# Performance work log

Measured on AMD Instinct MI355X. Metric: run time of the kernel, lower is better.

Reference implementation:

```python
import jax, jax.numpy as jnp
import numpy as np

DIM = 384
H_RES, W_RES = 56, 56
HEADS = 12
WS = 7          # window size
SS = 3          # shift size
N = WS * WS     # tokens per window
NW = (H_RES // WS) * (W_RES // WS)
EPS = 1e-5


def _rel_pos_index(ws):
    coords = np.stack(np.meshgrid(np.arange(ws), np.arange(ws), indexing='ij'))  # [2,ws,ws]
    cf = coords.reshape(2, -1)                      # [2, N]
    rc = (cf[:, :, None] - cf[:, None, :]).transpose(1, 2, 0)  # [N,N,2]
    rc[..., 0] += ws - 1
    rc[..., 1] += ws - 1
    rc[..., 0] *= 2 * ws - 1
    return rc.sum(-1)                               # [N,N] int


def _attn_mask(h, w, ws, ss):
    img = np.zeros((h, w))
    cnt = 0
    slices = (slice(0, -ws), slice(-ws, -ss), slice(-ss, None))
    for hs in slices:
        for wsl in slices:
            img[hs, wsl] = cnt
            cnt += 1
    mw = img.reshape(h // ws, ws, w // ws, ws).transpose(0, 2, 1, 3).reshape(-1, ws * ws)  # [nW,N]
    d = mw[:, None, :] - mw[:, :, None]
    return np.where(d != 0, -100.0, 0.0).astype(np.float32)  # [nW,N,N]


RPI = jnp.asarray(_rel_pos_index(WS).reshape(-1))          # [N*N]
ATTN_MASK = jnp.asarray(_attn_mask(H_RES, W_RES, WS, SS))  # [nW,N,N]


def _layernorm(x, g, b):
    mu = jnp.mean(x, axis=-1, keepdims=True)
    var = jnp.mean(jnp.square(x - mu), axis=-1, keepdims=True)
    return (x - mu) * jax.lax.rsqrt(var + EPS) * g + b


def setup_inputs() -> dict:
    key = jax.random.key(0)
    ks = jax.random.split(key, 8)
    s = 0.02
    return {
        'x': jax.random.normal(ks[0], (32, 1 + H_RES * W_RES, DIM), jnp.float32),
        'norm1_g': jnp.ones((DIM,), jnp.float32),
        'norm1_b': jnp.zeros((DIM,), jnp.float32),
        'qkv_w': jax.random.normal(ks[1], (DIM, 3 * DIM), jnp.float32) * s,
        'qkv_b': jnp.zeros((3 * DIM,), jnp.float32),
        'rpb_table': jax.random.normal(ks[2], ((2 * WS - 1) ** 2, HEADS), jnp.float32) * s,
        'proj_w': jax.random.normal(ks[3], (DIM, DIM), jnp.float32) * s,
        'proj_b': jnp.zeros((DIM,), jnp.float32),
        'norm2_g': jnp.ones((DIM,), jnp.float32),
        'norm2_b': jnp.zeros((DIM,), jnp.float32),
        'fc1_w': jax.random.normal(ks[4], (DIM, 4 * DIM), jnp.float32) * s,
        'fc1_b': jnp.zeros((4 * DIM,), jnp.float32),
        'fc2_w': jax.random.normal(ks[5], (4 * DIM, DIM), jnp.float32) * s,
        'fc2_b': jnp.zeros((DIM,), jnp.float32),
    }


def reference(x, norm1_g, norm1_b, qkv_w, qkv_b, rpb_table, proj_w, proj_b,
              norm2_g, norm2_b, fc1_w, fc1_b, fc2_w, fc2_b):
    B = x.shape[0]
    C = DIM
    hd = C // HEADS
    scale = hd ** -0.5

    time_token = x[:, :1, :]          # [B,1,C]
    img = x[:, 1:, :]                 # [B,H*W,C]
    shortcut = img

    h = _layernorm(img, norm1_g, norm1_b).reshape(B, H_RES, W_RES, C)
    h = jnp.roll(h, shift=(-SS, -SS), axis=(1, 2))  # cyclic shift

    # window partition -> [B*nW, N, C]
    xw = h.reshape(B, H_RES // WS, WS, W_RES // WS, WS, C)
    xw = xw.transpose(0, 1, 3, 2, 4, 5).reshape(-1, N, C)

    # window attention
    qkv = (xw @ qkv_w + qkv_b).reshape(-1, N, 3, HEADS, hd).transpose(2, 0, 3, 1, 4)
    q, k, v = qkv[0], qkv[1], qkv[2]                 # [B*nW, H, N, hd]
    attn = jnp.einsum('whnd,whmd->whnm', q * scale, k)
    bias = rpb_table[RPI].reshape(N, N, HEADS).transpose(2, 0, 1)  # [H,N,N]
    attn = attn + bias[None]
    attn = attn.reshape(B, NW, HEADS, N, N) + ATTN_MASK[None, :, None]
    attn = jax.nn.softmax(attn.reshape(-1, HEADS, N, N), axis=-1)
    out = jnp.einsum('whnm,whmd->wnhd', attn, v).reshape(-1, N, C)
    out = out @ proj_w + proj_b

    # window reverse -> [B,H,W,C]
    out = out.reshape(B, H_RES // WS, W_RES // WS, WS, WS, C)
    out = out.transpose(0, 1, 3, 2, 4, 5).reshape(B, H_RES, W_RES, C)
    out = jnp.roll(out, shift=(SS, SS), axis=(1, 2)).reshape(B, H_RES * W_RES, C)

    img = shortcut + out
    x = jnp.concatenate([time_token, img], axis=1)   # [B,1+H*W,C]
    x = _layernorm(x, norm2_g, norm2_b)
    hmlp = jax.nn.gelu(x @ fc1_w + fc1_b, approximate=False)
    x = x + (hmlp @ fc2_w + fc2_b)
    return x
```

## Files before the change

### kernel.cpp

```cpp
#include <hip/hip_runtime.h>
#include <hip/hip_bf16.h>

#define DIM 384
#define HEADS 12
#define NTOK 49
#define TOKENS 3137
#define M_ATTN 100352
#define M_FULL 100384
#define M_PAD  100480
#define SCALEQ 0.17677669529663687f

typedef __attribute__((ext_vector_type(8))) short s8v;
typedef __attribute__((ext_vector_type(4))) float f4v;
typedef unsigned short u16;

__device__ __forceinline__ float b2f(int s) {
  union { unsigned u; float f; } c; c.u = ((unsigned)(s & 0xffff)) << 16; return c.f;
}
__device__ __forceinline__ u16 f2b(float f) {
  __hip_bfloat16 h = __float2bfloat16(f);
  return *reinterpret_cast<u16*>(&h);
}
__device__ __forceinline__ void gload16(const void* g, void* l) {
  __builtin_amdgcn_global_load_lds((const __attribute__((address_space(1))) void*)g,
                                   (__attribute__((address_space(3))) void*)l, 16, 0, 0);
}
__device__ __forceinline__ float gelu_f(float val) {
  float u = __builtin_fmaf(0.0713548163f * val, val * val, 1.5957691216f * val);
  return val * __builtin_amdgcn_rcpf(1.0f + __expf(-u));
}
__device__ __forceinline__ size_t tidx(int tile, int KS, int rl, int c) {
  return ((size_t)(tile * KS + (c >> 6)) * 128 + rl) * 64
       + (((((c >> 3) & 7)) ^ (rl & 7)) << 3) + (c & 7);
}

__global__ void k_convert(const float* __restrict__ qkv_w, const float* __restrict__ qkv_b,
                          const float* __restrict__ proj_w, const float* __restrict__ fc1_w,
                          const float* __restrict__ fc2_w,
                          u16* __restrict__ wt_qkv, float* __restrict__ qkvb_s,
                          u16* __restrict__ wt_proj, u16* __restrict__ wt_fc1,
                          u16* __restrict__ wt_fc2) {
  int i = blockIdx.x * 256 + threadIdx.x;
  if (i < 1152 * 384) { int n = i / 384, k = i % 384;
    float v = qkv_w[(size_t)k * 1152 + n]; if (n < 384) v *= SCALEQ;
    wt_qkv[tidx(n >> 7, 6, n & 127, k)] = f2b(v); }
  if (i < 1152) qkvb_s[i] = qkv_b[i] * (i < 384 ? SCALEQ : 1.0f);
  if (i < 384 * 384) { int n = i / 384, k = i % 384;
    wt_proj[tidx(n >> 7, 6, n & 127, k)] = f2b(proj_w[(size_t)k * 384 + n]); }
  if (i < 1536 * 384) { int n = i / 384, k = i % 384;
    wt_fc1[tidx(n >> 7, 6, n & 127, k)] = f2b(fc1_w[(size_t)k * 1536 + n]); }
  if (i < 384 * 1536) { int n = i / 1536, k = i % 1536;
    wt_fc2[tidx(n >> 7, 24, n & 127, k)] = f2b(fc2_w[(size_t)k * 384 + n]); }
}

__global__ void k_addtab(const float* __restrict__ rpb, float* __restrict__ ADD) {
  int idx = blockIdx.x * 256 + threadIdx.x;
  if (idx >= 4 * HEADS * NTOK * NTOK) return;
  int j = idx % NTOK, t = idx / NTOK;
  int i = t % NTOK; t /= NTOK;
  int h = t % HEADS; int cls = t / HEADS;
  int ii = i / 7, jj = i % 7, ji = j / 7, j2 = j % 7;
  int rpi = (ii - ji + 6) * 13 + (jj - j2 + 6);
  float v = rpb[rpi * HEADS + h];
  int rh = (cls & 2) ? (ii < 4 ? 1 : 2) : 0;
  int rw = (cls & 1) ? (jj < 4 ? 1 : 2) : 0;
  int sh = (cls & 2) ? (ji < 4 ? 1 : 2) : 0;
  int sw = (cls & 1) ? (j2 < 4 ? 1 : 2) : 0;
  if (rh != sh || rw != sw) v -= 100.0f;
  ADD[idx] = v;
}

__global__ void k_ln1(const float* __restrict__ x, const float* __restrict__ g,
                      const float* __restrict__ b, u16* __restrict__ xwt, int t0) {
  int wid = threadIdx.x >> 6, lane = threadIdx.x & 63;
  int ml = blockIdx.x * 4 + wid;
  int t = t0 + ml;
  int bi = t / 3136, rem = t % 3136;
  int win = rem / NTOK, n = rem % NTOK;
  int wh = win >> 3, ww = win & 7, ii = n / 7, jj = n % 7;
  int h = (wh * 7 + ii + 3) % 56;
  int w = (ww * 7 + jj + 3) % 56;
  const float* src = x + ((size_t)bi * TOKENS + 1 + h * 56 + w) * DIM;
  float v[6];
  #pragma unroll
  for (int e = 0; e < 6; e++) v[e] = src[lane + e * 64];
  float s = v[0] + v[1] + v[2] + v[3] + v[4] + v[5];
  #pragma unroll
  for (int m = 1; m < 64; m <<= 1) s += __shfl_xor(s, m);
  float mu = s * (1.0f / 384.0f);
  float q = 0.f;
  #pragma unroll
  for (int e = 0; e < 6; e++) { float d = v[e] - mu; q += d * d; }
  #pragma unroll
  for (int m = 1; m < 64; m <<= 1) q += __shfl_xor(q, m);
  float rstd = rsqrtf(q * (1.0f / 384.0f) + 1e-5f);
  int tile = ml >> 7, rl = ml & 127;
  #pragma unroll
  for (int e = 0; e < 6; e++) {
    int c = lane + e * 64;
    xwt[tidx(tile, 6, rl, c)] = f2b((v[e] - mu) * rstd * g[c] + b[c]);
  }
}

template<int MODE>
__global__ __launch_bounds__(256) void k_gemm(
    const u16* __restrict__ At, const u16* __restrict__ Bt,
    const float* __restrict__ bias, u16* __restrict__ Cb,
    float* __restrict__ outp, const u16* __restrict__ residt,
    int N, int KT, int row_off) {
  __shared__ __align__(16) u16 As[2][128 * 64];
  __shared__ __align__(16) u16 Bs[2][128 * 64];
  int gx = gridDim.x;
  int lid = blockIdx.y * gx + blockIdx.x;
  int nwg = gx * gridDim.y;
  int q = nwg >> 3, r = nwg & 7;
  int xcd = lid & 7, loc = lid >> 3;
  int tile = (xcd < r ? xcd * (q + 1) : r * (q + 1) + (xcd - r) * q) + loc;
  int m0 = (tile / gx) * 128, n0 = (tile % gx) * 128;
  int t = threadIdx.x;
  int lane = t & 63, wave = t >> 6;
  int lo = lane & 15, hi = lane >> 4;
  int wr = (wave >> 1) * 64, wc = (wave & 1) * 64;
  const u16* Ag = At + ((size_t)(m0 >> 7) * KT) * 8192 + wave * 2048 + lane * 8;
  const u16* Bg = Bt + ((size_t)(n0 >> 7) * KT) * 8192 + wave * 2048 + lane * 8;
  f4v acc[4][4];
  #pragma unroll
  for (int m = 0; m < 4; m++)
    #pragma unroll
    for (int n = 0; n < 4; n++) acc[m][n] = (f4v)(0.0f);
#define STAGE(buf, kt) do {                                              \
    u16* al_ = As[buf] + wave * 2048;                                    \
    u16* bl_ = Bs[buf] + wave * 2048;                                    \
    _Pragma("unroll")                                                    \
    for (int g_ = 0; g_ < 4; g_++) {                                     \
      gload16(Ag + (size_t)(kt) * 8192 + g_ * 512, al_ + g_ * 512);      \
      gload16(Bg + (size_t)(kt) * 8192 + g_ * 512, bl_ + g_ * 512);      \
    } } while (0)
  STAGE(0, 0);
  for (int kt = 0; kt < KT; ++kt) {
    int c = kt & 1;
    if (kt + 1 < KT) {
      STAGE(1 - c, kt + 1);
      asm volatile("s_waitcnt vmcnt(8)" ::: "memory");
    } else {
      asm volatile("s_waitcnt vmcnt(0)" ::: "memory");
    }
    __builtin_amdgcn_s_barrier();
    __builtin_amdgcn_sched_barrier(0);
    s8v af[2][4], bfr[2][4];
    #pragma unroll
    for (int kk = 0; kk < 2; kk++) {
      #pragma unroll
      for (int m = 0; m < 4; m++) {
        int row = wr + m * 16 + lo;
        af[kk][m] = *(const s8v*)(As[c] + row * 64 + (((kk * 4 + hi) ^ (row & 7)) * 8));
      }
      #pragma unroll
      for (int n = 0; n < 4; n++) {
        int row = wc + n * 16 + lo;
        bfr[kk][n] = *(const s8v*)(Bs[c] + row * 64 + (((kk * 4 + hi) ^ (row & 7)) * 8));
      }
    }
    asm volatile("s_waitcnt lgkmcnt(0)" ::: "memory");
    __builtin_amdgcn_sched_barrier(0);
    __builtin_amdgcn_s_barrier();
    __builtin_amdgcn_sched_barrier(0);
    __builtin_amdgcn_s_setprio(1);
    #pragma unroll
    for (int kk = 0; kk < 2; kk++)
      #pragma unroll
      for (int m = 0; m < 4; m++)
        #pragma unroll
        for (int n = 0; n < 4; n++)
          acc[m][n] = __builtin_amdgcn_mfma_f32_16x16x32_bf16(af[kk][m], bfr[kk][n], acc[m][n], 0, 0, 0);
    __builtin_amdgcn_s_setprio(0);
  }
#undef STAGE
  #pragma unroll
  for (int m = 0; m < 4; m++) {
    #pragma unroll
    for (int n = 0; n < 4; n++) {
      int gcol = n0 + wc + n * 16 + lo;
      float bv = bias[gcol];
      #pragma unroll
      for (int r2 = 0; r2 < 4; r2++) {
        int lrow = wr + m * 16 + hi * 4 + r2;
        float val = acc[m][n][r2] + bv;
        if (MODE == 0) {
          Cb[(size_t)(m0 + lrow) * N + gcol] = f2b(val);
        } else if (MODE == 1) {
          Cb[tidx(m0 >> 7, 24, lrow, gcol)] = f2b(gelu_f(val));
        } else {
          int orow = m0 + lrow + row_off;
          if (orow < M_FULL) {
            float res = b2f(residt[tidx(orow >> 7, 6, orow & 127, gcol)]);
            outp[(size_t)orow * 384 + gcol] = val + res;
          }
        }
      }
    }
  }
}

__global__ __launch_bounds__(256) void k_attn2(const u16* __restrict__ qkv,
                                               const float* __restrict__ ADD,
                                               u16* __restrict__ aot, int win0) {
  __shared__ u16 PT[4][64][76];
  __shared__ u16 VT[4][32][76];
  int wid = threadIdx.x >> 6, lane = threadIdx.x & 63;
  int lo = lane & 15, hi = lane >> 4;
  int gw = blockIdx.x * 4 + wid;
  int win_l = gw / HEADS, h = gw % HEADS;
  int nw = (win0 + win_l) & 63;
  int wh = nw >> 3, ww = nw & 7;
  int cls = ((wh == 7) ? 2 : 0) + ((ww == 7) ? 1 : 0);
  size_t rowbase = (size_t)win_l * NTOK;
  u16 (*pt)[76] = PT[wid];
  u16 (*vt)[76] = VT[wid];

  int rcl[4];
  #pragma unroll
  for (int ti = 0; ti < 4; ti++) {
    int r = ti * 16 + lo;
    rcl[ti] = r < NTOK ? r : NTOK - 1;
  }
  int jrow = lane < NTOK ? lane : NTOK - 1;

  s8v af[4], bf[4];
  #pragma unroll
  for (int ti = 0; ti < 4; ti++) {
    af[ti] = *(const s8v*)(qkv + (rowbase + rcl[ti]) * 1152 + h * 32 + hi * 8);
    bf[ti] = *(const s8v*)(qkv + (rowbase + rcl[ti]) * 1152 + 384 + h * 32 + hi * 8);
  }
  f4v st[4][4];
  #pragma unroll
  for (int mi = 0; mi < 4; mi++)
    #pragma unroll
    for (int ni = 0; ni < 4; ni++)
      st[mi][ni] = __builtin_amdgcn_mfma_f32_16x16x32_bf16(af[mi], bf[ni], (f4v)(0.0f), 0, 0, 0);

  {
    const u16* vsrc = qkv + (rowbase + jrow) * 1152 + 768 + h * 32;
    #pragma unroll
    for (int d0 = 0; d0 < 32; d0 += 8) {
      s8v v = *(const s8v*)(vsrc + d0);
      #pragma unroll
      for (int e = 0; e < 8; e++) vt[d0 + e][lane] = (u16)v[e];
    }
  }

  const float* addb = ADD + ((size_t)cls * HEADS + h) * (NTOK * NTOK);
  #pragma unroll
  for (int mi = 0; mi < 4; mi++)
    #pragma unroll
    for (int ni = 0; ni < 4; ni++) {
      int jj = ni * 16 + lo;
      #pragma unroll
      for (int r = 0; r < 4; r++) {
        int i = mi * 16 + hi * 4 + r;
        if (jj < NTOK) {
          int ic = i < NTOK ? i : NTOK - 1;
          st[mi][ni][r] += addb[ic * NTOK + jj];
        } else st[mi][ni][r] = -1e30f;
      }
    }

  float invl[4][4];
  #pragma unroll
  for (int mi = 0; mi < 4; mi++)
    #pragma unroll
    for (int r = 0; r < 4; r++) {
      float m = fmaxf(fmaxf(st[mi][0][r], st[mi][1][r]), fmaxf(st[mi][2][r], st[mi][3][r]));
      #pragma unroll
      for (int msk = 1; msk < 16; msk <<= 1) m = fmaxf(m, __shfl_xor(m, msk));
      float s = 0.f;
      #pragma unroll
      for (int ni = 0; ni < 4; ni++) {
        float p = __expf(st[mi][ni][r] - m);
        st[mi][ni][r] = p;
        s += p;
      }
      #pragma unroll
      for (int msk = 1; msk < 16; msk <<= 1) s += __shfl_xor(s, msk);
      invl[mi][r] = 1.0f / s;
    }

  #pragma unroll
  for (int ni = 0; ni < 4; ni++)
    #pragma unroll
    for (int mi = 0; mi < 4; mi++) {
      ushort4 pk;
      pk.x = f2b(st[mi][ni][0]); pk.y = f2b(st[mi][ni][1]);
      pk.z = f2b(st[mi][ni][2]); pk.w = f2b(st[mi][ni][3]);
      *(ushort4*)(&pt[ni * 16 + lo][mi * 16 + hi * 4]) = pk;
    }

  f4v ot[4][2];
  #pragma unroll
  for (int mi = 0; mi < 4; mi++)
    #pragma unroll
    for (int dt = 0; dt < 2; dt++) ot[mi][dt] = (f4v)(0.0f);
  #pragma unroll
  for (int kt = 0; kt < 2; kt++) {
    s8v pa[4], vb[2];
    #pragma unroll
    for (int mi = 0; mi < 4; mi++) {
      s8v p;
      #pragma unroll
      for (int e = 0; e < 8; e++) p[e] = (short)pt[kt * 32 + hi * 8 + e][mi * 16 + lo];
      pa[mi] = p;
    }
    #pragma unroll
    for (int dt = 0; dt < 2; dt++) {
      short4 a = *(const short4*)(&vt[dt * 16 + lo][kt * 32 + hi * 8]);
      short4 b = *(const short4*)(&vt[dt * 16 + lo][kt * 32 + hi * 8 + 4]);
      s8v v; v[0] = a.x; v[1] = a.y; v[2] = a.z; v[3] = a.w;
             v[4] = b.x; v[5] = b.y; v[6] = b.z; v[7] = b.w;
      vb[dt] = v;
    }
    #pragma unroll
    for (int mi = 0; mi < 4; mi++)
      #pragma unroll
      for (int dt = 0; dt < 2; dt++)
        ot[mi][dt] = __builtin_amdgcn_mfma_f32_16x16x32_bf16(pa[mi], vb[dt], ot[mi][dt], 0, 0, 0);
  }

  #pragma unroll
  for (int mi = 0; mi < 4; mi++)
    #pragma unroll
    for (int r = 0; r < 4; r++) {
      int i = mi * 16 + hi * 4 + r;
      if (i < NTOK) {
        int row = (int)rowbase + i;
        int tile = row >> 7, rl = row & 127;
        aot[tidx(tile, 6, rl, h * 32 + lo)]      = f2b(ot[mi][0][r] * invl[mi][r]);
        aot[tidx(tile, 6, rl, h * 32 + 16 + lo)] = f2b(ot[mi][1][r] * invl[mi][r]);
      }
    }
}

__global__ void k_ln2(const float* __restrict__ x, const u16* __restrict__ proj,
                      const float* __restrict__ g, const float* __restrict__ b,
                      u16* __restrict__ x2bt) {
  int wid = threadIdx.x >> 6, lane = threadIdx.x & 63;
  int r = blockIdx.x * 4 + wid;
  int tile = r >> 7, rl = r & 127;
  if (r >= M_FULL) {
    u16 z = f2b(0.0f);
    #pragma unroll
    for (int e = 0; e < 6; e++) x2bt[tidx(tile, 6, rl, lane + e * 64)] = z;
    return;
  }
  int bi = r / TOKENS, tk = r % TOKENS;
  const float* xs = x + (size_t)r * DIM;
  float v[6];
  if (tk == 0) {
    #pragma unroll
    for (int e = 0; e < 6; e++) v[e] = xs[lane + e * 64];
  } else {
    int p = tk - 1, hh = p / 56, wp = p % 56;
    int a = (hh + 53) % 56, bw = (wp + 53) % 56;
    int wh = a / 7, ii = a % 7, w2 = bw / 7, jj = bw % 7;
    size_t prow = ((size_t)bi * 64 + wh * 8 + w2) * NTOK + ii * 7 + jj;
    const u16* ps = proj + prow * DIM;
    #pragma unroll
    for (int e = 0; e < 6; e++) v[e] = xs[lane + e * 64] + b2f(ps[lane + e * 64]);
  }
  float s = v[0] + v[1] + v[2] + v[3] + v[4] + v[5];
  #pragma unroll
  for (int m = 1; m < 64; m <<= 1) s += __shfl_xor(s, m);
  float mu = s * (1.0f / 384.0f);
  float q = 0.f;
  #pragma unroll
  for (int e = 0; e < 6; e++) { float d = v[e] - mu; q += d * d; }
  #pragma unroll
  for (int m = 1; m < 64; m <<= 1) q += __shfl_xor(q, m);
  float rstd = rsqrtf(q * (1.0f / 384.0f) + 1e-5f);
  #pragma unroll
  for (int e = 0; e < 6; e++) {
    int c = lane + e * 64;
    x2bt[tidx(tile, 6, rl, c)] = f2b((v[e] - mu) * rstd * g[c] + b[c]);
  }
}

extern "C" void kernel_launch(void* const* d_in, const int* in_sizes, int n_in,
                              void* d_out, int out_size, void* d_ws, size_t ws_size,
                              hipStream_t stream) {
  const float* x      = (const float*)d_in[0];
  const float* n1g    = (const float*)d_in[1];
  const float* n1b    = (const float*)d_in[2];
  const float* qkv_w  = (const float*)d_in[3];
  const float* qkv_b  = (const float*)d_in[4];
  const float* rpb    = (const float*)d_in[5];
  const float* proj_w = (const float*)d_in[6];
  const float* proj_b = (const float*)d_in[7];
  const float* n2g    = (const float*)d_in[8];
  const float* n2b    = (const float*)d_in[9];
  const float* fc1_w  = (const float*)d_in[10];
  const float* fc1_b  = (const float*)d_in[11];
  const float* fc2_w  = (const float*)d_in[12];
  const float* fc2_b  = (const float*)d_in[13];
  float* outp = (float*)d_out;

  auto al = [](size_t v) { return (v + 255) & ~(size_t)255; };
  size_t base = al(884736) + al(294912) + al(1179648) + al(1179648) + al(4608)
              + al(460992) + al((size_t)M_PAD * 768);
  const int cand[3][2] = {{4, 4}, {8, 8}, {16, 16}};
  int NC1 = 16, NC2 = 16;
  for (int ci = 0; ci < 3; ci++) {
    int c1 = cand[ci][0], c2 = cand[ci][1];
    size_t cm = M_ATTN / c1;
    size_t cb_ = (785 + c2 - 1) / c2;
    size_t region = (size_t)M_ATTN * 768;
    size_t fc1b = cb_ * 24 * 8192 * 2;
    if (fc1b > region) region = fc1b;
    size_t tot = base + 2 * al(cm * 768) + al(cm * 2304) + al(region);
    if (tot <= ws_size) { NC1 = c1; NC2 = c2; break; }
  }
  char* p = (char*)d_ws;
  auto take = [&](size_t bytes) { char* r = p; p += al(bytes); return r; };
  u16* wt_qkv  = (u16*)take(884736);
  u16* wt_proj = (u16*)take(294912);
  u16* wt_fc1  = (u16*)take(1179648);
  u16* wt_fc2  = (u16*)take(1179648);
  float* qkvb_s = (float*)take(4608);
  float* ADDt   = (float*)take(460992);
  u16* X2Bt = (u16*)take((size_t)M_PAD * 768);
  int chunkM = M_ATTN / NC1;
  u16* XWt  = (u16*)take((size_t)chunkM * 768);
  u16* QKV  = (u16*)take((size_t)chunkM * 2304);
  u16* AOt  = (u16*)take((size_t)chunkM * 768);
  int cb = (785 + NC2 - 1) / NC2;
  size_t region = (size_t)M_ATTN * 768;
  size_t fc1b = (size_t)cb * 24 * 8192 * 2;
  if (fc1b > region) region = fc1b;
  u16* PROJ = (u16*)take(region);
  u16* FC1t = PROJ;

  k_convert<<<2304, 256, 0, stream>>>(qkv_w, qkv_b, proj_w, fc1_w, fc2_w,
                                      wt_qkv, qkvb_s, wt_proj, wt_fc1, wt_fc2);
  k_addtab<<<451, 256, 0, stream>>>(rpb, ADDt);
  int chunkWin = chunkM / NTOK;
  for (int c = 0; c < NC1; c++) {
    int t0 = c * chunkM;
    k_ln1<<<chunkM / 4, 256, 0, stream>>>(x, n1g, n1b, XWt, t0);
    k_gemm<0><<<dim3(9, chunkM / 128), 256, 0, stream>>>(XWt, wt_qkv, qkvb_s, QKV,
                                                         nullptr, nullptr, 1152, 6, 0);
    k_attn2<<<chunkWin * HEADS / 4, 256, 0, stream>>>(QKV, ADDt, AOt, c * chunkWin);
    k_gemm<0><<<dim3(3, chunkM / 128), 256, 0, stream>>>(AOt, wt_proj, proj_b,
                                                         PROJ + (size_t)t0 * DIM,
                                                         nullptr, nullptr, 384, 6, 0);
  }
  k_ln2<<<M_PAD / 4, 256, 0, stream>>>(x, PROJ, n2g, n2b, X2Bt);
  for (int c = 0; c < NC2; c++) {
    int rb0 = c * cb;
    int nb = 785 - rb0; if (nb > cb) nb = cb; if (nb <= 0) break;
    k_gemm<1><<<dim3(12, nb), 256, 0, stream>>>(X2Bt + (size_t)rb0 * 128 * 384, wt_fc1,
                                                fc1_b, FC1t, nullptr, nullptr, 1536, 6, 0);
    k_gemm<2><<<dim3(3, nb), 256, 0, stream>>>(FC1t, wt_fc2, fc2_b, nullptr, outp, X2Bt,
                                               384, 24, rb0 * 128);
  }
}
```

Before: 1.048 ms.

## Replace 128x128 GEMM tiles with 256x256 tiles using 512-thread blocks

```diff
diff --git a/kernel.cpp b/kernel.cpp
--- a/kernel.cpp
+++ b/kernel.cpp
@@ -7,7 +7,7 @@
 #define TOKENS 3137
 #define M_ATTN 100352
 #define M_FULL 100384
-#define M_PAD  100480
+#define M_PAD2 100608
 #define SCALEQ 0.17677669529663687f
 
 typedef __attribute__((ext_vector_type(8))) short s8v;
@@ -35,22 +35,33 @@
 }
 
 __global__ void k_convert(const float* __restrict__ qkv_w, const float* __restrict__ qkv_b,
-                          const float* __restrict__ proj_w, const float* __restrict__ fc1_w,
-                          const float* __restrict__ fc2_w,
+                          const float* __restrict__ proj_w, const float* __restrict__ proj_b,
+                          const float* __restrict__ fc1_w, const float* __restrict__ fc1_b,
+                          const float* __restrict__ fc2_w, const float* __restrict__ fc2_b,
                           u16* __restrict__ wt_qkv, float* __restrict__ qkvb_s,
-                          u16* __restrict__ wt_proj, u16* __restrict__ wt_fc1,
-                          u16* __restrict__ wt_fc2) {
+                          u16* __restrict__ wt_proj, float* __restrict__ projb_s,
+                          u16* __restrict__ wt_fc1, float* __restrict__ fc1b_s,
+                          u16* __restrict__ wt_fc2, float* __restrict__ fc2b_s) {
   int i = blockIdx.x * 256 + threadIdx.x;
   if (i < 1152 * 384) { int n = i / 384, k = i % 384;
     float v = qkv_w[(size_t)k * 1152 + n]; if (n < 384) v *= SCALEQ;
     wt_qkv[tidx(n >> 7, 6, n & 127, k)] = f2b(v); }
-  if (i < 1152) qkvb_s[i] = qkv_b[i] * (i < 384 ? SCALEQ : 1.0f);
+  if (i < 128 * 384) { int n = 1152 + i / 384, k = i % 384;
+    wt_qkv[tidx(n >> 7, 6, n & 127, k)] = 0; }
+  if (i < 1280) qkvb_s[i] = (i < 1152) ? qkv_b[i] * (i < 384 ? SCALEQ : 1.0f) : 0.0f;
   if (i < 384 * 384) { int n = i / 384, k = i % 384;
     wt_proj[tidx(n >> 7, 6, n & 127, k)] = f2b(proj_w[(size_t)k * 384 + n]); }
+  if (i < 128 * 384) { int n = 384 + i / 384, k = i % 384;
+    wt_proj[tidx(n >> 7, 6, n & 127, k)] = 0; }
+  if (i < 512) projb_s[i] = (i < 384) ? proj_b[i] : 0.0f;
   if (i < 1536 * 384) { int n = i / 384, k = i % 384;
     wt_fc1[tidx(n >> 7, 6, n & 127, k)] = f2b(fc1_w[(size_t)k * 1536 + n]); }
+  if (i < 1536) fc1b_s[i] = fc1_b[i];
   if (i < 384 * 1536) { int n = i / 1536, k = i % 1536;
     wt_fc2[tidx(n >> 7, 24, n & 127, k)] = f2b(fc2_w[(size_t)k * 384 + n]); }
+  if (i < 128 * 1536) { int n = 384 + i / 1536, k = i % 1536;
+    wt_fc2[tidx(n >> 7, 24, n & 127, k)] = 0; }
+  if (i < 512) fc2b_s[i] = (i < 384) ? fc2_b[i] : 0.0f;
 }
 
 __global__ void k_addtab(const float* __restrict__ rpb, float* __restrict__ ADD) {
@@ -103,103 +114,103 @@
 }
 
 template<int MODE>
-__global__ __launch_bounds__(256) void k_gemm(
+__global__ __launch_bounds__(512, 2) void k_gemm256(
     const u16* __restrict__ At, const u16* __restrict__ Bt,
     const float* __restrict__ bias, u16* __restrict__ Cb,
     float* __restrict__ outp, const u16* __restrict__ residt,
-    int N, int KT, int row_off) {
-  __shared__ __align__(16) u16 As[2][128 * 64];
-  __shared__ __align__(16) u16 Bs[2][128 * 64];
+    int Nreal, int KT, int row_off) {
+  __shared__ __align__(16) u16 Ls[2][4][8192];
   int gx = gridDim.x;
   int lid = blockIdx.y * gx + blockIdx.x;
   int nwg = gx * gridDim.y;
   int q = nwg >> 3, r = nwg & 7;
   int xcd = lid & 7, loc = lid >> 3;
   int tile = (xcd < r ? xcd * (q + 1) : r * (q + 1) + (xcd - r) * q) + loc;
-  int m0 = (tile / gx) * 128, n0 = (tile % gx) * 128;
-  int t = threadIdx.x;
-  int lane = t & 63, wave = t >> 6;
+  int m0 = (tile / gx) * 256, n0 = (tile % gx) * 256;
+  int tid = threadIdx.x;
+  int wid = tid >> 6, lane = tid & 63;
   int lo = lane & 15, hi = lane >> 4;
-  int wr = (wave >> 1) * 64, wc = (wave & 1) * 64;
-  const u16* Ag = At + ((size_t)(m0 >> 7) * KT) * 8192 + wave * 2048 + lane * 8;
-  const u16* Bg = Bt + ((size_t)(n0 >> 7) * KT) * 8192 + wave * 2048 + lane * 8;
-  f4v acc[4][4];
-  #pragma unroll
-  for (int m = 0; m < 4; m++)
-    #pragma unroll
-    for (int n = 0; n < 4; n++) acc[m][n] = (f4v)(0.0f);
-#define STAGE(buf, kt) do {                                              \
-    u16* al_ = As[buf] + wave * 2048;                                    \
-    u16* bl_ = Bs[buf] + wave * 2048;                                    \
+  int wm = wid >> 2, wn = wid & 3;
+  int cidx = wid >> 1, half = wid & 1;
+  const u16* gsrc = (cidx < 2)
+      ? At + ((size_t)((m0 >> 7) + cidx) * KT) * 8192
+      : Bt + ((size_t)((n0 >> 7) + (cidx - 2)) * KT) * 8192;
+  gsrc += half * 4096 + lane * 8;
+  f4v acc[8][4];
+  #pragma unroll
+  for (int mi = 0; mi < 8; mi++)
+    #pragma unroll
+    for (int ni = 0; ni < 4; ni++) acc[mi][ni] = (f4v)(0.0f);
+#define STG(buf, kt) do {                                                \
+    u16* d_ = &Ls[buf][cidx][half * 4096];                               \
+    const u16* s_ = gsrc + (size_t)(kt) * 8192;                          \
     _Pragma("unroll")                                                    \
-    for (int g_ = 0; g_ < 4; g_++) {                                     \
-      gload16(Ag + (size_t)(kt) * 8192 + g_ * 512, al_ + g_ * 512);      \
-      gload16(Bg + (size_t)(kt) * 8192 + g_ * 512, bl_ + g_ * 512);      \
-    } } while (0)
-  STAGE(0, 0);
+    for (int g_ = 0; g_ < 8; g_++) gload16(s_ + g_ * 512, d_ + g_ * 512);\
+  } while (0)
+  STG(0, 0);
   for (int kt = 0; kt < KT; ++kt) {
     int c = kt & 1;
     if (kt + 1 < KT) {
-      STAGE(1 - c, kt + 1);
+      STG(1 - c, kt + 1);
       asm volatile("s_waitcnt vmcnt(8)" ::: "memory");
     } else {
       asm volatile("s_waitcnt vmcnt(0)" ::: "memory");
     }
     __builtin_amdgcn_s_barrier();
     __builtin_amdgcn_sched_barrier(0);
-    s8v af[2][4], bfr[2][4];
     #pragma unroll
     for (int kk = 0; kk < 2; kk++) {
-      #pragma unroll
-      for (int m = 0; m < 4; m++) {
-        int row = wr + m * 16 + lo;
-        af[kk][m] = *(const s8v*)(As[c] + row * 64 + (((kk * 4 + hi) ^ (row & 7)) * 8));
-      }
-      #pragma unroll
-      for (int n = 0; n < 4; n++) {
-        int row = wc + n * 16 + lo;
-        bfr[kk][n] = *(const s8v*)(Bs[c] + row * 64 + (((kk * 4 + hi) ^ (row & 7)) * 8));
-      }
-    }
-    asm volatile("s_waitcnt lgkmcnt(0)" ::: "memory");
-    __builtin_amdgcn_sched_barrier(0);
-    __builtin_amdgcn_s_barrier();
-    __builtin_amdgcn_sched_barrier(0);
-    __builtin_amdgcn_s_setprio(1);
-    #pragma unroll
-    for (int kk = 0; kk < 2; kk++)
-      #pragma unroll
-      for (int m = 0; m < 4; m++)
+      int kk4 = kk * 4;
+      s8v af[8], bf[4];
+      #pragma unroll
+      for (int mi = 0; mi < 8; mi++) {
+        int rl = mi * 16 + lo;
+        af[mi] = *(const s8v*)(&Ls[c][wm][rl * 64 + (((kk4 + hi) ^ (rl & 7)) << 3)]);
+      }
+      #pragma unroll
+      for (int ni = 0; ni < 4; ni++) {
+        int rb = (wn & 1) * 64 + ni * 16 + lo;
+        bf[ni] = *(const s8v*)(&Ls[c][2 + (wn >> 1)][rb * 64 + (((kk4 + hi) ^ (rb & 7)) << 3)]);
+      }
+      asm volatile("s_waitcnt lgkmcnt(0)" ::: "memory");
+      __builtin_amdgcn_sched_barrier(0);
+      if (kk == 1) {
+        __builtin_amdgcn_s_barrier();
+        __builtin_amdgcn_sched_barrier(0);
+      }
+      __builtin_amdgcn_s_setprio(1);
+      #pragma unroll
+      for (int mi = 0; mi < 8; mi++)
         #pragma unroll
-        for (int n = 0; n < 4; n++)
-          acc[m][n] = __builtin_amdgcn_mfma_f32_16x16x32_bf16(af[kk][m], bfr[kk][n], acc[m][n], 0, 0, 0);
-    __builtin_amdgcn_s_setprio(0);
-  }
-#undef STAGE
-  #pragma unroll
-  for (int m = 0; m < 4; m++) {
-    #pragma unroll
-    for (int n = 0; n < 4; n++) {
-      int gcol = n0 + wc + n * 16 + lo;
+        for (int ni = 0; ni < 4; ni++)
+          acc[mi][ni] = __builtin_amdgcn_mfma_f32_16x16x32_bf16(af[mi], bf[ni], acc[mi][ni], 0, 0, 0);
+      __builtin_amdgcn_s_setprio(0);
+    }
+  }
+#undef STG
+  #pragma unroll
+  for (int mi = 0; mi < 8; mi++)
+    #pragma unroll
+    for (int ni = 0; ni < 4; ni++) {
+      int gcol = n0 + wn * 64 + ni * 16 + lo;
       float bv = bias[gcol];
       #pragma unroll
       for (int r2 = 0; r2 < 4; r2++) {
-        int lrow = wr + m * 16 + hi * 4 + r2;
-        float val = acc[m][n][r2] + bv;
+        int grow = m0 + wm * 128 + mi * 16 + hi * 4 + r2;
+        float val = acc[mi][ni][r2] + bv;
         if (MODE == 0) {
-          Cb[(size_t)(m0 + lrow) * N + gcol] = f2b(val);
+          if (gcol < Nreal) Cb[(size_t)grow * Nreal + gcol] = f2b(val);
         } else if (MODE == 1) {
-          Cb[tidx(m0 >> 7, 24, lrow, gcol)] = f2b(gelu_f(val));
+          Cb[tidx(grow >> 7, 24, grow & 127, gcol)] = f2b(gelu_f(val));
         } else {
-          int orow = m0 + lrow + row_off;
-          if (orow < M_FULL) {
+          int orow = grow + row_off;
+          if (orow < M_FULL && gcol < Nreal) {
             float res = b2f(residt[tidx(orow >> 7, 6, orow & 127, gcol)]);
             outp[(size_t)orow * 384 + gcol] = val + res;
           }
         }
       }
     }
-  }
 }
 
 __global__ __launch_bounds__(256) void k_attn2(const u16* __restrict__ qkv,
@@ -403,61 +414,68 @@
   float* outp = (float*)d_out;
 
   auto al = [](size_t v) { return (v + 255) & ~(size_t)255; };
-  size_t base = al(884736) + al(294912) + al(1179648) + al(1179648) + al(4608)
-              + al(460992) + al((size_t)M_PAD * 768);
-  const int cand[3][2] = {{4, 4}, {8, 8}, {16, 16}};
-  int NC1 = 16, NC2 = 16;
-  for (int ci = 0; ci < 3; ci++) {
+  size_t base = al(983040) + al(393216) + al(1179648) + al(1572864)
+              + al(5120) + al(2048) + al(6144) + al(2048)
+              + al(460992) + al((size_t)M_PAD2 * 768);
+  const int cand[4][2] = {{4, 4}, {4, 8}, {8, 8}, {8, 16}};
+  int NC1 = 8, NC2 = 16;
+  for (int ci = 0; ci < 4; ci++) {
     int c1 = cand[ci][0], c2 = cand[ci][1];
     size_t cm = M_ATTN / c1;
-    size_t cb_ = (785 + c2 - 1) / c2;
+    int ct = (393 + c2 - 1) / c2;
     size_t region = (size_t)M_ATTN * 768;
-    size_t fc1b = cb_ * 24 * 8192 * 2;
+    size_t fc1b = (size_t)ct * 786432;
     if (fc1b > region) region = fc1b;
     size_t tot = base + 2 * al(cm * 768) + al(cm * 2304) + al(region);
     if (tot <= ws_size) { NC1 = c1; NC2 = c2; break; }
   }
   char* p = (char*)d_ws;
   auto take = [&](size_t bytes) { char* r = p; p += al(bytes); return r; };
-  u16* wt_qkv  = (u16*)take(884736);
-  u16* wt_proj = (u16*)take(294912);
+  u16* wt_qkv  = (u16*)take(983040);
+  u16* wt_proj = (u16*)take(393216);
   u16* wt_fc1  = (u16*)take(1179648);
-  u16* wt_fc2  = (u16*)take(1179648);
-  float* qkvb_s = (float*)take(4608);
+  u16* wt_fc2  = (u16*)take(1572864);
+  float* qkvb_s = (float*)take(5120);
+  float* projb_s = (float*)take(2048);
+  float* fc1b_s = (float*)take(6144);
+  float* fc2b_s = (float*)take(2048);
   float* ADDt   = (float*)take(460992);
-  u16* X2Bt = (u16*)take((size_t)M_PAD * 768);
+  u16* X2Bt = (u16*)take((size_t)M_PAD2 * 768);
   int chunkM = M_ATTN / NC1;
   u16* XWt  = (u16*)take((size_t)chunkM * 768);
   u16* QKV  = (u16*)take((size_t)chunkM * 2304);
   u16* AOt  = (u16*)take((size_t)chunkM * 768);
-  int cb = (785 + NC2 - 1) / NC2;
+  int ct = (393 + NC2 - 1) / NC2;
   size_t region = (size_t)M_ATTN * 768;
-  size_t fc1b = (size_t)cb * 24 * 8192 * 2;
+  size_t fc1b = (size_t)ct * 786432;
   if (fc1b > region) region = fc1b;
   u16* PROJ = (u16*)take(region);
   u16* FC1t = PROJ;
 
-  k_convert<<<2304, 256, 0, stream>>>(qkv_w, qkv_b, proj_w, fc1_w, fc2_w,
-                                      wt_qkv, qkvb_s, wt_proj, wt_fc1, wt_fc2);
+  k_convert<<<2304, 256, 0, stream>>>(qkv_w, qkv_b, proj_w, proj_b, fc1_w, fc1_b,
+                                      fc2_w, fc2_b, wt_qkv, qkvb_s, wt_proj, projb_s,
+                                      wt_fc1, fc1b_s, wt_fc2, fc2b_s);
   k_addtab<<<451, 256, 0, stream>>>(rpb, ADDt);
   int chunkWin = chunkM / NTOK;
+  int mt1 = chunkM / 256;
   for (int c = 0; c < NC1; c++) {
     int t0 = c * chunkM;
     k_ln1<<<chunkM / 4, 256, 0, stream>>>(x, n1g, n1b, XWt, t0);
-    k_gemm<0><<<dim3(9, chunkM / 128), 256, 0, stream>>>(XWt, wt_qkv, qkvb_s, QKV,
-                                                         nullptr, nullptr, 1152, 6, 0);
+    k_gemm256<0><<<dim3(5, mt1), 512, 0, stream>>>(XWt, wt_qkv, qkvb_s, QKV,
+                                                   nullptr, nullptr, 1152, 6, 0);
     k_attn2<<<chunkWin * HEADS / 4, 256, 0, stream>>>(QKV, ADDt, AOt, c * chunkWin);
-    k_gemm<0><<<dim3(3, chunkM / 128), 256, 0, stream>>>(AOt, wt_proj, proj_b,
-                                                         PROJ + (size_t)t0 * DIM,
-                                                         nullptr, nullptr, 384, 6, 0);
-  }
-  k_ln2<<<M_PAD / 4, 256, 0, stream>>>(x, PROJ, n2g, n2b, X2Bt);
+    k_gemm256<0><<<dim3(2, mt1), 512, 0, stream>>>(AOt, wt_proj, projb_s,
+                                                   PROJ + (size_t)t0 * DIM,
+                                                   nullptr, nullptr, 384, 6, 0);
+  }
+  k_ln2<<<M_PAD2 / 4, 256, 0, stream>>>(x, PROJ, n2g, n2b, X2Bt);
   for (int c = 0; c < NC2; c++) {
-    int rb0 = c * cb;
-    int nb = 785 - rb0; if (nb > cb) nb = cb; if (nb <= 0) break;
-    k_gemm<1><<<dim3(12, nb), 256, 0, stream>>>(X2Bt + (size_t)rb0 * 128 * 384, wt_fc1,
-                                                fc1_b, FC1t, nullptr, nullptr, 1536, 6, 0);
-    k_gemm<2><<<dim3(3, nb), 256, 0, stream>>>(FC1t, wt_fc2, fc2_b, nullptr, outp, X2Bt,
-                                               384, 24, rb0 * 128);
-  }
-}
+    int tb0 = c * ct;
+    int nt = 393 - tb0; if (nt > ct) nt = ct; if (nt <= 0) break;
+    k_gemm256<1><<<dim3(6, nt), 512, 0, stream>>>(
+        X2Bt + (size_t)(tb0 * 2) * 6 * 8192, wt_fc1, fc1b_s, FC1t,
+        nullptr, nullptr, 1536, 6, 0);
+    k_gemm256<2><<<dim3(2, nt), 512, 0, stream>>>(
+        FC1t, wt_fc2, fc2b_s, nullptr, outp, X2Bt, 384, 24, tb0 * 256);
+  }
+}
```

Result: faster. 1.013 ms (-3.3%).
